# Performance work log

Measured on AMD Instinct MI355X. Metric: run time of the kernel, lower is better.

## Reference

```python
import jax, jax.numpy as jnp
import numpy as np

S = 8192          # total tokens (8 images x 1024 patches)
DIM = 1280        # hidden_size
H = 16            # num_heads
DH = DIM // H     # head_dim = 80
N_SEG = 8         # number of image segments (equal-length)


def setup_inputs() -> dict:
    key = jax.random.key(0)
    ks = jax.random.split(key, 8)
    hidden_states = jax.random.normal(ks[0], (S, DIM), dtype=jnp.float32)
    ang = jax.random.uniform(ks[1], (S, DH), dtype=jnp.float32) * (2.0 * np.pi)
    cos = jnp.cos(ang)
    sin = jnp.sin(ang)
    cu_seqlens = (jnp.arange(N_SEG + 1, dtype=jnp.int32) * (S // N_SEG))
    qkv_w = jax.random.normal(ks[2], (3 * DIM, DIM), dtype=jnp.float32) * 0.02
    qkv_b = jax.random.normal(ks[3], (3 * DIM,), dtype=jnp.float32) * 0.02
    proj_w = jax.random.normal(ks[4], (DIM, DIM), dtype=jnp.float32) * 0.02
    proj_b = jax.random.normal(ks[5], (DIM,), dtype=jnp.float32) * 0.02
    return {
        "hidden_states": hidden_states,
        "cos": cos,
        "sin": sin,
        "qkv_w": qkv_w,
        "qkv_b": qkv_b,
        "proj_w": proj_w,
        "proj_b": proj_b,
        "cu_seqlens": cu_seqlens,
    }


def _rotate_half(x):
    d = x.shape[-1] // 2
    return jnp.concatenate([-x[..., d:], x[..., :d]], axis=-1)


def reference(hidden_states, cos, sin, qkv_w, qkv_b, proj_w, proj_b, cu_seqlens):
    s, dim = hidden_states.shape
    dh = cos.shape[-1]
    h = dim // dh
    n_seg = cu_seqlens.shape[0] - 1  # static; segments are equal-length
    L = s // n_seg
    scale = dh ** -0.5

    # fused QKV projection: [S, 3, H, DH]
    qkv = (hidden_states @ qkv_w.T + qkv_b).reshape(s, 3, h, dh)
    q, k, v = qkv[:, 0], qkv[:, 1], qkv[:, 2]

    # RoPE (fp32, broadcast cos/sin over heads)
    cos_b = cos[:, None, :].astype(jnp.float32)
    sin_b = sin[:, None, :].astype(jnp.float32)
    qf, kf = q.astype(jnp.float32), k.astype(jnp.float32)
    q = (qf * cos_b + _rotate_half(qf) * sin_b).astype(q.dtype)
    k = (kf * cos_b + _rotate_half(kf) * sin_b).astype(k.dtype)

    # per-segment (block-diagonal) attention: reshape to [n_seg, L, H, DH]
    qs = q.reshape(n_seg, L, h, dh)
    ks = k.reshape(n_seg, L, h, dh)
    vs = v.reshape(n_seg, L, h, dh)
    scores = jnp.einsum("glhd,gmhd->ghlm", qs, ks) * scale
    attn = jax.nn.softmax(scores, axis=-1)
    out = jnp.einsum("ghlm,gmhd->glhd", attn, vs).reshape(s, dim)
    return out @ proj_w.T + proj_b
```

## Files before the change

### kernel.cpp

```cpp
#include <hip/hip_runtime.h>
#include <hip/hip_bf16.h>
#include <stdint.h>

typedef unsigned short u16;
typedef unsigned int u32;
typedef __attribute__((ext_vector_type(8))) short short8;
typedef __attribute__((ext_vector_type(4))) float f32x4;

#define DEV __device__ __forceinline__

constexpr int S = 8192;
constexpr int DIM = 1280;
constexpr int H = 16;
constexpr int DH = 80;
constexpr int LSEG = 1024;
constexpr int QKVN = 3 * DIM;
constexpr float SCALE = 0.11180339887498949f * 1.4426950408889634f;

DEV u16 f2bf(float f) {
  u32 u = __float_as_uint(f);
  return (u16)((u + 0x7FFFu + ((u >> 16) & 1u)) >> 16);
}
DEV float bf2f(u16 h) { return __uint_as_float(((u32)h) << 16); }
DEV u32 pkbf(float a, float b) {
  __hip_bfloat162 t = __float22bfloat162_rn(float2{a, b});
  u32 r; __builtin_memcpy(&r, &t, 4); return r;
}

DEV void glds16(const void* g, void* l) {
  __builtin_amdgcn_global_load_lds((__attribute__((address_space(1))) void*)g,
                                   (__attribute__((address_space(3))) void*)l,
                                   16, 0, 0);
}
DEV f32x4 mfma16(short8 a, short8 b, f32x4 c) {
  return __builtin_amdgcn_mfma_f32_16x16x32_bf16(a, b, c, 0, 0, 0);
}

__global__ __launch_bounds__(256) void cvt_kernel(
    const float* __restrict__ X, const float* __restrict__ Wq,
    const float* __restrict__ Wp, u16* __restrict__ Xb,
    u16* __restrict__ Wqb, u16* __restrict__ Wpb) {
  size_t i = ((size_t)blockIdx.x * 256 + threadIdx.x) * 4;
  const size_t n1 = (size_t)S * DIM;
  const size_t n2 = (size_t)QKVN * DIM;
  const size_t n3 = (size_t)DIM * DIM;
  const float* src; u16* dst; size_t off;
  if (i < n1)                { src = X;  dst = Xb;  off = i; }
  else if (i < n1 + n2)      { src = Wq; dst = Wqb; off = i - n1; }
  else if (i < n1 + n2 + n3) { src = Wp; dst = Wpb; off = i - n1 - n2; }
  else return;
  float4 v = *(const float4*)(src + off);
  ushort4 r;
  r.x = f2bf(v.x); r.y = f2bf(v.y); r.z = f2bf(v.z); r.w = f2bf(v.w);
  *(ushort4*)(dst + off) = r;
}

__global__ __launch_bounds__(256) void rope_kernel(
    const u16* __restrict__ QKV, const float* __restrict__ cosp,
    const float* __restrict__ sinp, u16* __restrict__ Qp, u16* __restrict__ Kp) {
  int idx = blockIdx.x * 256 + threadIdx.x;
  int c = idx % 5;
  int sh = idx / 5;
  int s = sh >> 4, h = sh & 15;
  const size_t gbase = (size_t)s * QKVN + h * DH + c * 8;
  const size_t pbase = (size_t)sh * 96 + c * 8;
  short8 q0 = *(const short8*)&QKV[gbase];
  short8 q1 = *(const short8*)&QKV[gbase + 40];
  short8 k0 = *(const short8*)&QKV[gbase + DIM];
  short8 k1 = *(const short8*)&QKV[gbase + DIM + 40];
  float4 ca0 = *(const float4*)&cosp[s * DH + c * 8];
  float4 ca1 = *(const float4*)&cosp[s * DH + c * 8 + 4];
  float4 cb0 = *(const float4*)&cosp[s * DH + c * 8 + 40];
  float4 cb1 = *(const float4*)&cosp[s * DH + c * 8 + 44];
  float4 sa0 = *(const float4*)&sinp[s * DH + c * 8];
  float4 sa1 = *(const float4*)&sinp[s * DH + c * 8 + 4];
  float4 sb0 = *(const float4*)&sinp[s * DH + c * 8 + 40];
  float4 sb1 = *(const float4*)&sinp[s * DH + c * 8 + 44];
  float ca[8] = {ca0.x, ca0.y, ca0.z, ca0.w, ca1.x, ca1.y, ca1.z, ca1.w};
  float cb[8] = {cb0.x, cb0.y, cb0.z, cb0.w, cb1.x, cb1.y, cb1.z, cb1.w};
  float sa[8] = {sa0.x, sa0.y, sa0.z, sa0.w, sa1.x, sa1.y, sa1.z, sa1.w};
  float sb[8] = {sb0.x, sb0.y, sb0.z, sb0.w, sb1.x, sb1.y, sb1.z, sb1.w};
  short8 qo0, qo1, ko0, ko1;
#pragma unroll
  for (int j = 0; j < 8; j++) {
    float qa = bf2f((u16)q0[j]), qb = bf2f((u16)q1[j]);
    float ka = bf2f((u16)k0[j]), kb = bf2f((u16)k1[j]);
    qo0[j] = (short)f2bf((qa * ca[j] - qb * sa[j]) * SCALE);
    qo1[j] = (short)f2bf((qb * cb[j] + qa * sb[j]) * SCALE);
    ko0[j] = (short)f2bf(ka * ca[j] - kb * sa[j]);
    ko1[j] = (short)f2bf(kb * cb[j] + ka * sb[j]);
  }
  *(short8*)&Qp[pbase]      = qo0;
  *(short8*)&Qp[pbase + 40] = qo1;
  *(short8*)&Kp[pbase]      = ko0;
  *(short8*)&Kp[pbase + 40] = ko1;
  if (c == 0) {
    short8 z = {};
    *(short8*)&Qp[pbase + 80] = z; *(short8*)&Qp[pbase + 88] = z;
    *(short8*)&Kp[pbase + 80] = z; *(short8*)&Kp[pbase + 88] = z;
  }
}

__global__ __launch_bounds__(256) void vtrans_kernel(
    const u16* __restrict__ QKV, u16* __restrict__ Vt) {
  __shared__ u16 Ls[64 * 88];
  const int s0 = blockIdx.x * 64, h = blockIdx.y;
  const int tid = threadIdx.x;
  for (int cc = tid; cc < 640; cc += 256) {
    int row = cc / 10, c = cc % 10;
    short8 v = *(const short8*)&QKV[(size_t)(s0 + row) * QKVN + 2 * DIM + h * 80 + c * 8];
    *(short8*)&Ls[row * 88 + c * 8] = v;
  }
  __syncthreads();
  for (int cc = tid; cc < 640; cc += 256) {
    int d = cc / 8, sc = cc % 8;
    u16 tmp[8];
#pragma unroll
    for (int j = 0; j < 8; j++) {
      int op = sc * 8 + j;
      int key = ((op & 3) << 4) + (op >> 2);
      tmp[j] = Ls[key * 88 + d];
    }
    *(short8*)&Vt[(size_t)(h * 80 + d) * S + s0 + sc * 8] = *(short8*)tmp;
  }
}

template <bool OUT_F32>
__global__ __launch_bounds__(512, 2) void gemm_bt(
    const u16* __restrict__ A, const u16* __restrict__ B,
    const float* __restrict__ bias, void* __restrict__ C, int K, int N) {
  __shared__ u16 As[2][2][8192];
  __shared__ u16 Bs[2][2][8192];
  const int ntn = N >> 8;
  const int q = gridDim.x >> 3;
  const int widx = (blockIdx.x & 7) * q + (blockIdx.x >> 3);
  const int m0 = (widx / ntn) << 8;
  const int n0 = (widx % ntn) << 8;
  const int tid = threadIdx.x;
  const int w = tid >> 6, lane = tid & 63;
  const int quad = lane >> 4, l16 = lane & 15;
  const int wm = w >> 2, wn = w & 3;

  const int rowoff = w * 8 + (lane >> 3);
  const int coloff = ((lane & 7) ^ (lane >> 3)) * 8;
  const u16* pa0 = A + (size_t)(m0 + rowoff) * K + coloff;
  const u16* pa1 = A + (size_t)(m0 + 128 + rowoff) * K + coloff;
  const u16* pb0 = B + (size_t)(n0 + rowoff) * K + coloff;
  const u16* pb1 = B + (size_t)(n0 + 128 + rowoff) * K + coloff;
  const size_t j64 = (size_t)64 * K;

#define STG(P, DST, kk) do { \
    glds16((P) + (kk), &(DST)[w * 512]); \
    glds16((P) + j64 + (kk), &(DST)[4096 + w * 512]); } while (0)

  const int aro = (wm * 16 + l16) * 64;
  const int bro = (wn * 16 + l16) * 64;
  const int kc0 = ((quad) ^ (l16 & 7)) * 8;
  const int kc1 = ((4 + quad) ^ (l16 & 7)) * 8;

  f32x4 acc[8][4] = {};
  short8 af[4][2], bf0[2][2], bf1[2][2];
  const int NT = K >> 6;

  STG(pa0, As[0][0], 0); STG(pb0, Bs[0][0], 0);
  STG(pa1, As[0][1], 0); STG(pb1, Bs[0][1], 0);
  STG(pa0, As[1][0], 64); STG(pb0, Bs[1][0], 64);
  asm volatile("s_waitcnt vmcnt(4)" ::: "memory");
  asm volatile("s_barrier" ::: "memory");

  for (int t = 0; t < NT; ++t) {
    const int b = t & 1;
    const int kk1 = (t + 1) << 6, kk2 = (t + 2) << 6;
#pragma unroll
    for (int i = 0; i < 4; i++) {
      af[i][0] = *(const short8*)&As[b][0][aro + i * 2048 + kc0];
      af[i][1] = *(const short8*)&As[b][0][aro + i * 2048 + kc1];
    }
#pragma unroll
    for (int jj = 0; jj < 2; jj++) {
      bf0[jj][0] = *(const short8*)&Bs[b][0][bro + jj * 4096 + kc0];
      bf0[jj][1] = *(const short8*)&Bs[b][0][bro + jj * 4096 + kc1];
    }
    if (t + 1 < NT) { STG(pa1, As[b ^ 1][1], kk1); STG(pb1, Bs[b ^ 1][1], kk1); }
    asm volatile("s_barrier" ::: "memory");
    __builtin_amdgcn_s_setprio(1);
#pragma unroll
    for (int ks = 0; ks < 2; ks++)
#pragma unroll
      for (int i = 0; i < 4; i++)
#pragma unroll
        for (int jj = 0; jj < 2; jj++)
          acc[i][jj] = mfma16(af[i][ks], bf0[jj][ks], acc[i][jj]);
    __builtin_amdgcn_s_setprio(0);
    asm volatile("s_barrier" ::: "memory");
#pragma unroll
    for (int jj = 0; jj < 2; jj++) {
      bf1[jj][0] = *(const short8*)&Bs[b][1][bro + jj * 4096 + kc0];
      bf1[jj][1] = *(const short8*)&Bs[b][1][bro + jj * 4096 + kc1];
    }
    if (t + 2 < NT) STG(pa0, As[b][0], kk2);
    asm volatile("s_barrier" ::: "memory");
    __builtin_amdgcn_s_setprio(1);
#pragma unroll
    for (int ks = 0; ks < 2; ks++)
#pragma unroll
      for (int i = 0; i < 4; i++)
#pragma unroll
        for (int jj = 0; jj < 2; jj++)
          acc[i][2 + jj] = mfma16(af[i][ks], bf1[jj][ks], acc[i][2 + jj]);
    __builtin_amdgcn_s_setprio(0);
    asm volatile("s_barrier" ::: "memory");
#pragma unroll
    for (int i = 0; i < 4; i++) {
      af[i][0] = *(const short8*)&As[b][1][aro + i * 2048 + kc0];
      af[i][1] = *(const short8*)&As[b][1][aro + i * 2048 + kc1];
    }
    if (t + 2 < NT) STG(pb0, Bs[b][0], kk2);
    asm volatile("s_barrier" ::: "memory");
    __builtin_amdgcn_s_setprio(1);
#pragma unroll
    for (int ks = 0; ks < 2; ks++)
#pragma unroll
      for (int i = 0; i < 4; i++)
#pragma unroll
        for (int jj = 0; jj < 2; jj++)
          acc[4 + i][jj] = mfma16(af[i][ks], bf0[jj][ks], acc[4 + i][jj]);
    __builtin_amdgcn_s_setprio(0);
    asm volatile("s_barrier" ::: "memory");
    __builtin_amdgcn_s_setprio(1);
#pragma unroll
    for (int ks = 0; ks < 2; ks++)
#pragma unroll
      for (int i = 0; i < 4; i++)
#pragma unroll
        for (int jj = 0; jj < 2; jj++)
          acc[4 + i][2 + jj] = mfma16(af[i][ks], bf1[jj][ks], acc[4 + i][2 + jj]);
    __builtin_amdgcn_s_setprio(0);
    if (t < NT - 2)       asm volatile("s_waitcnt vmcnt(4)" ::: "memory");
    else if (t == NT - 2) asm volatile("s_waitcnt vmcnt(0)" ::: "memory");
    asm volatile("s_barrier" ::: "memory");
  }
#undef STG
#pragma unroll
  for (int nf = 0; nf < 4; nf++) {
    int col = n0 + nf * 64 + wn * 16 + l16;
    float bv = bias[col];
#pragma unroll
    for (int mf = 0; mf < 8; mf++) {
#pragma unroll
      for (int r = 0; r < 4; r++) {
        int row = m0 + mf * 32 + wm * 16 + quad * 4 + r;
        float v = acc[mf][nf][r] + bv;
        if (OUT_F32) ((float*)C)[(size_t)row * N + col] = v;
        else         ((u16*)C)[(size_t)row * N + col] = f2bf(v);
      }
    }
  }
}

__global__ __launch_bounds__(256, 2) void attn_kernel(
    const u16* __restrict__ Qp, const u16* __restrict__ Kp,
    const u16* __restrict__ Vt, u16* __restrict__ O) {
  __shared__ u16 Ks[2][64 * 104];
  __shared__ u16 Vs[2][86 * 72];
  __shared__ u16 Ps[4][16 * 72];
  const int bid = blockIdx.x;
  const int phi = bid & 7, qt = (bid >> 3) & 7, pj = bid >> 6;
  const int p = pj * 8 + phi;
  const int g = p >> 4, h = p & 15;
  const int tid = threadIdx.x;
  const int w = tid >> 6, lane = tid & 63;
  const int quad = lane >> 4, l16 = lane & 15;

  short8 aq[2][3];
  const size_t qbase = ((size_t)(g * LSEG + qt * 128 + w * 32 + l16)) * 1536 + h * 96;
#pragma unroll
  for (int mt = 0; mt < 2; mt++)
#pragma unroll
    for (int ks = 0; ks < 3; ks++)
      aq[mt][ks] = *(const short8*)&Qp[qbase + (size_t)mt * 16 * 1536 + ks * 32 + quad * 8];

  const u16* gp[7]; u16* lp0[7]; u16* lp1[7]; int stp[7]; bool act[7];
#pragma unroll
  for (int i = 0; i < 7; i++) {
    int c = w + 4 * i;
    act[i] = (c < 25);
    int cc = act[i] ? c : 0;
    if (cc < 13) {
      int idx = cc * 64 + lane;
      int key = idx / 13, rc = idx % 13;
      int col = rc * 8; if (col >= 96) col = 0;
      gp[i] = Kp + (size_t)(g * LSEG + key) * 1536 + h * 96 + col;
      stp[i] = 64 * 1536;
      lp0[i] = &Ks[0][cc * 512]; lp1[i] = &Ks[1][cc * 512];
    } else {
      int cv = cc - 13;
      int idx = cv * 64 + lane;
      int d = idx / 9, rc = idx % 9;
      int col = rc * 8; if (col >= 64) col = 0;
      if (d >= 80) d = 0;
      gp[i] = Vt + (size_t)(h * 80 + d) * S + g * LSEG + col;
      stp[i] = 64;
      lp0[i] = &Vs[0][cv * 512]; lp1[i] = &Vs[1][cv * 512];
    }
  }
#pragma unroll
  for (int i = 0; i < 7; i++)
    if (act[i]) { glds16(gp[i], lp0[i]); gp[i] += stp[i]; }

  f32x4 o[2][5] = {};
  float lr[2][4] = {};
  u16* psw = &Ps[w][0];

  for (int kb = 0; kb < LSEG / 64; kb++) {
    const int b = kb & 1;
    __syncthreads();
    if (kb < LSEG / 64 - 1) {
      if (b == 0) {
#pragma unroll
        for (int i = 0; i < 7; i++)
          if (act[i]) { glds16(gp[i], lp1[i]); gp[i] += stp[i]; }
      } else {
#pragma unroll
        for (int i = 0; i < 7; i++)
          if (act[i]) { glds16(gp[i], lp0[i]); gp[i] += stp[i]; }
      }
    }
    f32x4 s[2][4] = {};
#pragma unroll
    for (int ks = 0; ks < 3; ks++) {
      short8 bk[4];
#pragma unroll
      for (int nt = 0; nt < 4; nt++)
        bk[nt] = *(const short8*)&Ks[b][(nt * 16 + l16) * 104 + ks * 32 + quad * 8];
#pragma unroll
      for (int mt = 0; mt < 2; mt++)
#pragma unroll
        for (int nt = 0; nt < 4; nt++)
          s[mt][nt] = mfma16(aq[mt][ks], bk[nt], s[mt][nt]);
    }
    short8 vb[5][2];
#pragma unroll
    for (int t = 0; t < 5; t++)
#pragma unroll
      for (int u = 0; u < 2; u++)
        vb[t][u] = *(const short8*)&Vs[b][(t * 16 + l16) * 72 + u * 32 + quad * 8];
#pragma unroll
    for (int mt = 0; mt < 2; mt++) {
#pragma unroll
      for (int r = 0; r < 4; r++) {
        float p0 = __builtin_amdgcn_exp2f(s[mt][0][r]);
        float p1 = __builtin_amdgcn_exp2f(s[mt][1][r]);
        float p2 = __builtin_amdgcn_exp2f(s[mt][2][r]);
        float p3 = __builtin_amdgcn_exp2f(s[mt][3][r]);
        lr[mt][r] += (p0 + p1) + (p2 + p3);
        int row = quad * 4 + r;
        uint2 pk; pk.x = pkbf(p0, p1); pk.y = pkbf(p2, p3);
        *(uint2*)&psw[row * 72 + l16 * 4] = pk;
      }
      short8 pa0 = *(const short8*)&psw[l16 * 72 + quad * 8];
      short8 pa1 = *(const short8*)&psw[l16 * 72 + 32 + quad * 8];
#pragma unroll
      for (int t = 0; t < 5; t++)
        o[mt][t] = mfma16(pa0, vb[t][0], o[mt][t]);
#pragma unroll
      for (int t = 0; t < 5; t++)
        o[mt][t] = mfma16(pa1, vb[t][1], o[mt][t]);
    }
  }
#pragma unroll
  for (int mt = 0; mt < 2; mt++)
#pragma unroll
    for (int r = 0; r < 4; r++) {
      float t = lr[mt][r];
#pragma unroll
      for (int off = 8; off >= 1; off >>= 1) t += __shfl_xor(t, off, 16);
      float inv = 1.f / t;
      int srow = g * LSEG + qt * 128 + w * 32 + mt * 16 + quad * 4 + r;
#pragma unroll
      for (int tt = 0; tt < 5; tt++)
        O[(size_t)srow * DIM + h * DH + tt * 16 + l16] = f2bf(o[mt][tt][r] * inv);
    }
}

extern "C" void kernel_launch(void* const* d_in, const int* in_sizes, int n_in,
                              void* d_out, int out_size, void* d_ws, size_t ws_size,
                              hipStream_t stream) {
  const float* X     = (const float*)d_in[0];
  const float* cosp  = (const float*)d_in[1];
  const float* sinp  = (const float*)d_in[2];
  const float* qkvw  = (const float*)d_in[3];
  const float* qkvb  = (const float*)d_in[4];
  const float* projw = (const float*)d_in[5];
  const float* projb = (const float*)d_in[6];
  float* out = (float*)d_out;

  u16* Xb   = (u16*)d_ws;
  u16* Wqb  = Xb   + (size_t)S * DIM;
  u16* Wpb  = Wqb  + (size_t)QKVN * DIM;
  u16* QKVb = Wpb  + (size_t)DIM * DIM;
  u16* Kp   = QKVb + (size_t)S * QKVN;
  u16* Vt   = Kp   + (size_t)S * H * 96;
  u16* Qp   = Xb;
  u16* AOb  = QKVb;

  cvt_kernel<<<16640, 256, 0, stream>>>(X, qkvw, projw, Xb, Wqb, Wpb);
  gemm_bt<false><<<(S / 256) * (QKVN / 256), 512, 0, stream>>>(Xb, Wqb, qkvb, QKVb, DIM, QKVN);
  rope_kernel<<<(S * H * 5) / 256, 256, 0, stream>>>(QKVb, cosp, sinp, Qp, Kp);
  vtrans_kernel<<<dim3(S / 64, H), 256, 0, stream>>>(QKVb, Vt);
  attn_kernel<<<1024, 256, 0, stream>>>(Qp, Kp, Vt, AOb);
  gemm_bt<true><<<(S / 256) * (DIM / 256), 512, 0, stream>>>(AOb, Wpb, projb, out, DIM, DIM);
}
```

Baseline: 332.7 us.

## Restructure GEMM LDS prefetch schedule with finer waitcnts and sched barriers

Result: faster. 325.2 us (-2.2%).

```diff
diff --git a/kernel.cpp b/kernel.cpp
--- a/kernel.cpp
+++ b/kernel.cpp
@@ -152,6 +152,8 @@
 #define STG(P, DST, kk) do { \
     glds16((P) + (kk), &(DST)[w * 512]); \
     glds16((P) + j64 + (kk), &(DST)[4096 + w * 512]); } while (0)
+#define BARR()  __builtin_amdgcn_s_barrier()
+#define SCHED0() __builtin_amdgcn_sched_barrier(0)
 
   const int aro = (wm * 16 + l16) * 64;
   const int bro = (wn * 16 + l16) * 64;
@@ -163,14 +165,14 @@
   const int NT = K >> 6;
 
   STG(pa0, As[0][0], 0); STG(pb0, Bs[0][0], 0);
-  STG(pa1, As[0][1], 0); STG(pb1, Bs[0][1], 0);
-  STG(pa0, As[1][0], 64); STG(pb0, Bs[1][0], 64);
-  asm volatile("s_waitcnt vmcnt(4)" ::: "memory");
-  asm volatile("s_barrier" ::: "memory");
+  STG(pb1, Bs[0][1], 0); STG(pa1, As[0][1], 0);
+  asm volatile("s_waitcnt vmcnt(4)");
+  BARR();
 
   for (int t = 0; t < NT; ++t) {
     const int b = t & 1;
-    const int kk1 = (t + 1) << 6, kk2 = (t + 2) << 6;
+    const int kk = (t + 1) << 6;
+    const bool pf = (t + 1 < NT);
 #pragma unroll
     for (int i = 0; i < 4; i++) {
       af[i][0] = *(const short8*)&As[b][0][aro + i * 2048 + kc0];
@@ -181,8 +183,11 @@
       bf0[jj][0] = *(const short8*)&Bs[b][0][bro + jj * 4096 + kc0];
       bf0[jj][1] = *(const short8*)&Bs[b][0][bro + jj * 4096 + kc1];
     }
-    if (t + 1 < NT) { STG(pa1, As[b ^ 1][1], kk1); STG(pb1, Bs[b ^ 1][1], kk1); }
-    asm volatile("s_barrier" ::: "memory");
+    if (pf) { STG(pa0, As[b ^ 1][0], kk); STG(pb0, Bs[b ^ 1][0], kk); }
+    asm volatile("s_waitcnt lgkmcnt(8)");
+    BARR();
+    asm volatile("s_waitcnt lgkmcnt(0)");
+    SCHED0();
     __builtin_amdgcn_s_setprio(1);
 #pragma unroll
     for (int ks = 0; ks < 2; ks++)
@@ -192,14 +197,20 @@
         for (int jj = 0; jj < 2; jj++)
           acc[i][jj] = mfma16(af[i][ks], bf0[jj][ks], acc[i][jj]);
     __builtin_amdgcn_s_setprio(0);
-    asm volatile("s_barrier" ::: "memory");
+    SCHED0();
+    if (t < NT - 1) asm volatile("s_waitcnt vmcnt(6)");
+    else            asm volatile("s_waitcnt vmcnt(2)");
+    SCHED0();
+    BARR();
 #pragma unroll
     for (int jj = 0; jj < 2; jj++) {
       bf1[jj][0] = *(const short8*)&Bs[b][1][bro + jj * 4096 + kc0];
       bf1[jj][1] = *(const short8*)&Bs[b][1][bro + jj * 4096 + kc1];
     }
-    if (t + 2 < NT) STG(pa0, As[b][0], kk2);
-    asm volatile("s_barrier" ::: "memory");
+    if (pf) STG(pb1, Bs[b ^ 1][1], kk);
+    BARR();
+    asm volatile("s_waitcnt lgkmcnt(0)");
+    SCHED0();
     __builtin_amdgcn_s_setprio(1);
 #pragma unroll
     for (int ks = 0; ks < 2; ks++)
@@ -209,14 +220,20 @@
         for (int jj = 0; jj < 2; jj++)
           acc[i][2 + jj] = mfma16(af[i][ks], bf1[jj][ks], acc[i][2 + jj]);
     __builtin_amdgcn_s_setprio(0);
-    asm volatile("s_barrier" ::: "memory");
+    SCHED0();
+    if (t < NT - 1) asm volatile("s_waitcnt vmcnt(6)");
+    else            asm volatile("s_waitcnt vmcnt(0)");
+    SCHED0();
+    BARR();
 #pragma unroll
     for (int i = 0; i < 4; i++) {
       af[i][0] = *(const short8*)&As[b][1][aro + i * 2048 + kc0];
       af[i][1] = *(const short8*)&As[b][1][aro + i * 2048 + kc1];
     }
-    if (t + 2 < NT) STG(pb0, Bs[b][0], kk2);
-    asm volatile("s_barrier" ::: "memory");
+    if (pf) STG(pa1, As[b ^ 1][1], kk);
+    BARR();
+    asm volatile("s_waitcnt lgkmcnt(0)");
+    SCHED0();
     __builtin_amdgcn_s_setprio(1);
 #pragma unroll
     for (int ks = 0; ks < 2; ks++)
@@ -226,7 +243,10 @@
         for (int jj = 0; jj < 2; jj++)
           acc[4 + i][jj] = mfma16(af[i][ks], bf0[jj][ks], acc[4 + i][jj]);
     __builtin_amdgcn_s_setprio(0);
-    asm volatile("s_barrier" ::: "memory");
+    SCHED0();
+    if (pf) asm volatile("s_waitcnt vmcnt(4)");
+    SCHED0();
+    BARR();
     __builtin_amdgcn_s_setprio(1);
 #pragma unroll
     for (int ks = 0; ks < 2; ks++)
@@ -236,11 +256,10 @@
         for (int jj = 0; jj < 2; jj++)
           acc[4 + i][2 + jj] = mfma16(af[i][ks], bf1[jj][ks], acc[4 + i][2 + jj]);
     __builtin_amdgcn_s_setprio(0);
-    if (t < NT - 2)       asm volatile("s_waitcnt vmcnt(4)" ::: "memory");
-    else if (t == NT - 2) asm volatile("s_waitcnt vmcnt(0)" ::: "memory");
-    asm volatile("s_barrier" ::: "memory");
   }
 #undef STG
+#undef BARR
+#undef SCHED0
 #pragma unroll
   for (int nf = 0; nf < 4; nf++) {
     int col = n0 + nf * 64 + wn * 16 + l16;
```

## Simplify GEMM pipeline to whole-tile double buffering with one barrier per step

Applied to the files above, without the earlier changes.

Result: slower. 346.0 us (+4.0%).

```diff
diff --git a/kernel.cpp b/kernel.cpp
--- a/kernel.cpp
+++ b/kernel.cpp
@@ -152,6 +152,7 @@
 #define STG(P, DST, kk) do { \
     glds16((P) + (kk), &(DST)[w * 512]); \
     glds16((P) + j64 + (kk), &(DST)[4096 + w * 512]); } while (0)
+#define BARR()  __builtin_amdgcn_s_barrier()
 
   const int aro = (wm * 16 + l16) * 64;
   const int bro = (wn * 16 + l16) * 64;
@@ -163,14 +164,17 @@
   const int NT = K >> 6;
 
   STG(pa0, As[0][0], 0); STG(pb0, Bs[0][0], 0);
-  STG(pa1, As[0][1], 0); STG(pb1, Bs[0][1], 0);
-  STG(pa0, As[1][0], 64); STG(pb0, Bs[1][0], 64);
-  asm volatile("s_waitcnt vmcnt(4)" ::: "memory");
-  asm volatile("s_barrier" ::: "memory");
+  STG(pb1, Bs[0][1], 0); STG(pa1, As[0][1], 0);
+  asm volatile("s_waitcnt vmcnt(0)");
+  BARR();
 
   for (int t = 0; t < NT; ++t) {
     const int b = t & 1;
-    const int kk1 = (t + 1) << 6, kk2 = (t + 2) << 6;
+    const int kk = (t + 1) << 6;
+    if (t + 1 < NT) {
+      STG(pa0, As[b ^ 1][0], kk); STG(pb0, Bs[b ^ 1][0], kk);
+      STG(pb1, Bs[b ^ 1][1], kk); STG(pa1, As[b ^ 1][1], kk);
+    }
 #pragma unroll
     for (int i = 0; i < 4; i++) {
       af[i][0] = *(const short8*)&As[b][0][aro + i * 2048 + kc0];
@@ -181,8 +185,6 @@
       bf0[jj][0] = *(const short8*)&Bs[b][0][bro + jj * 4096 + kc0];
       bf0[jj][1] = *(const short8*)&Bs[b][0][bro + jj * 4096 + kc1];
     }
-    if (t + 1 < NT) { STG(pa1, As[b ^ 1][1], kk1); STG(pb1, Bs[b ^ 1][1], kk1); }
-    asm volatile("s_barrier" ::: "memory");
     __builtin_amdgcn_s_setprio(1);
 #pragma unroll
     for (int ks = 0; ks < 2; ks++)
@@ -192,14 +194,11 @@
         for (int jj = 0; jj < 2; jj++)
           acc[i][jj] = mfma16(af[i][ks], bf0[jj][ks], acc[i][jj]);
     __builtin_amdgcn_s_setprio(0);
-    asm volatile("s_barrier" ::: "memory");
 #pragma unroll
     for (int jj = 0; jj < 2; jj++) {
       bf1[jj][0] = *(const short8*)&Bs[b][1][bro + jj * 4096 + kc0];
       bf1[jj][1] = *(const short8*)&Bs[b][1][bro + jj * 4096 + kc1];
     }
-    if (t + 2 < NT) STG(pa0, As[b][0], kk2);
-    asm volatile("s_barrier" ::: "memory");
     __builtin_amdgcn_s_setprio(1);
 #pragma unroll
     for (int ks = 0; ks < 2; ks++)
@@ -209,14 +208,11 @@
         for (int jj = 0; jj < 2; jj++)
           acc[i][2 + jj] = mfma16(af[i][ks], bf1[jj][ks], acc[i][2 + jj]);
     __builtin_amdgcn_s_setprio(0);
-    asm volatile("s_barrier" ::: "memory");
 #pragma unroll
     for (int i = 0; i < 4; i++) {
       af[i][0] = *(const short8*)&As[b][1][aro + i * 2048 + kc0];
       af[i][1] = *(const short8*)&As[b][1][aro + i * 2048 + kc1];
     }
-    if (t + 2 < NT) STG(pb0, Bs[b][0], kk2);
-    asm volatile("s_barrier" ::: "memory");
     __builtin_amdgcn_s_setprio(1);
 #pragma unroll
     for (int ks = 0; ks < 2; ks++)
@@ -225,9 +221,6 @@
 #pragma unroll
         for (int jj = 0; jj < 2; jj++)
           acc[4 + i][jj] = mfma16(af[i][ks], bf0[jj][ks], acc[4 + i][jj]);
-    __builtin_amdgcn_s_setprio(0);
-    asm volatile("s_barrier" ::: "memory");
-    __builtin_amdgcn_s_setprio(1);
 #pragma unroll
     for (int ks = 0; ks < 2; ks++)
 #pragma unroll
@@ -236,11 +229,11 @@
         for (int jj = 0; jj < 2; jj++)
           acc[4 + i][2 + jj] = mfma16(af[i][ks], bf1[jj][ks], acc[4 + i][2 + jj]);
     __builtin_amdgcn_s_setprio(0);
-    if (t < NT - 2)       asm volatile("s_waitcnt vmcnt(4)" ::: "memory");
-    else if (t == NT - 2) asm volatile("s_waitcnt vmcnt(0)" ::: "memory");
-    asm volatile("s_barrier" ::: "memory");
+    asm volatile("s_waitcnt vmcnt(0)");
+    BARR();
   }
 #undef STG
+#undef BARR
 #pragma unroll
   for (int nf = 0; nf < 4; nf++) {
     int col = n0 + nf * 64 + wn * 16 + l16;
```
